# Kernel optimization log

Measured on AMD Instinct MI355X. Metric: run time of the kernel, lower is better.

## Reference

```python
import jax, jax.numpy as jnp
import numpy as np

N_NODES = 100000
N_EDGES = 3200000
IN_CH = 32
OUT_CH = 32
DIM = 2
KSIZE = 3  # per pseudo dimension -> num_kernels = 9


def setup_inputs() -> dict:
    key = jax.random.key(0)
    k1, k2, k3, k4, k5, k6 = jax.random.split(key, 6)
    x = jax.random.normal(k1, (N_NODES, IN_CH), dtype=jnp.float32)
    pseudo = jax.random.uniform(k2, (N_EDGES, DIM), dtype=jnp.float32)
    weight = jax.random.normal(k3, (KSIZE * KSIZE, IN_CH, OUT_CH), dtype=jnp.float32) / np.sqrt(IN_CH)
    root_w = jax.random.normal(k4, (OUT_CH, IN_CH), dtype=jnp.float32) / np.sqrt(IN_CH)
    root_b = jax.random.normal(k5, (OUT_CH,), dtype=jnp.float32) * 0.01
    edge_index = jax.random.randint(k6, (2, N_EDGES), 0, N_NODES, dtype=jnp.int64)
    return {"x": x, "pseudo": pseudo, "weight": weight, "root_w": root_w,
            "root_b": root_b, "edge_index": edge_index}


def _basis(pseudo):
    # degree-1 B-spline (hat) basis per dim, outer product across dims -> [E, K^dim]
    p = jnp.clip(pseudo, 0.0, 1.0)  # [E, dim]
    grid = jnp.linspace(0.0, 1.0, KSIZE, dtype=p.dtype)  # [K]
    dist = jnp.abs(p[:, :, None] - grid[None, None, :])  # [E, dim, K]
    b = jnp.maximum(1.0 - dist * (KSIZE - 1), 0.0)  # [E, dim, K]
    basis = jnp.einsum('ea,eb->eab', b[:, 0], b[:, 1])  # [E, K, K]
    return basis.reshape(p.shape[0], -1)  # [E, K*K]


def reference(x, pseudo, weight, root_w, root_b, edge_index):
    row, col = edge_index[0], edge_index[1]
    basis = _basis(pseudo)  # [E, K]
    # gather + basis-weighted contraction -> per-edge messages [E, out]
    messages = jnp.einsum('ek,ei,kio->eo', basis, x[row], weight)
    out = jnp.zeros((x.shape[0], weight.shape[2]), dtype=x.dtype).at[col].add(messages)
    # mean aggregation: divide by in-degree (clamped to >= 1)
    degree = jnp.zeros((x.shape[0],), dtype=x.dtype).at[col].add(jnp.ones_like(col, dtype=x.dtype))
    out = out / jnp.maximum(degree, 1.0)[:, None]
    # root linear (torch nn.Linear: x @ W.T + b)
    out = out + x @ root_w.T + root_b
    return out
```

## Files before the change

kernel.cpp:

```cpp
#include <hip/hip_runtime.h>
#include <hip/hip_bf16.h>

#define N_NODES 100000
#define N_EDGES 3200000
#define CH 32
#define NK 9
#define KTOT 320
#define RS 328

#define BNODES 128
#define NBUCK ((N_NODES + BNODES - 1) / BNODES)
#define CURS_PAD 16
#define MAXB 4800
#define CHE 12288
#define NCHUNK ((N_EDGES + CHE - 1) / CHE)

typedef __hip_bfloat16 bf16;
typedef unsigned short u16;
typedef __attribute__((ext_vector_type(8))) short bf16x8;
typedef __attribute__((ext_vector_type(4))) float f32x4;

__global__ __launch_bounds__(256) void prep_kernel(const float* __restrict__ x,
                                                   const float* __restrict__ w,
                                                   const float* __restrict__ rw,
                                                   bf16* __restrict__ xb,
                                                   bf16* __restrict__ Bg) {
    int idx = blockIdx.x * 256 + threadIdx.x;
    if (idx < N_NODES * CH / 4) {
        float4 v = ((const float4*)x)[idx];
        union { bf16 h[4]; uint2 u; } pk;
        pk.h[0] = __float2bfloat16(v.x);
        pk.h[1] = __float2bfloat16(v.y);
        pk.h[2] = __float2bfloat16(v.z);
        pk.h[3] = __float2bfloat16(v.w);
        ((uint2*)xb)[idx] = pk.u;
    }
    if (idx < NK * CH * CH) {
        int kk = idx >> 5, o = idx & 31;
        Bg[o * RS + kk] = __float2bfloat16(w[idx]);
    }
    if (idx < CH * CH) {
        int o = idx >> 5, i = idx & 31;
        Bg[o * RS + 288 + i] = __float2bfloat16(rw[idx]);
    }
}

__global__ __launch_bounds__(256) void bhist_kernel(const int* __restrict__ ei_col,
                                                    int* __restrict__ hist) {
    __shared__ int h[NBUCK];
    for (int j = threadIdx.x; j < NBUCK; j += 256) h[j] = 0;
    __syncthreads();
    const int4* c4 = (const int4*)ei_col;
    int stride = gridDim.x * 256;
    for (int e = blockIdx.x * 256 + threadIdx.x; e < N_EDGES / 4; e += stride) {
        int4 v = c4[e];
        atomicAdd(&h[v.x >> 7], 1);
        atomicAdd(&h[v.y >> 7], 1);
        atomicAdd(&h[v.z >> 7], 1);
        atomicAdd(&h[v.w >> 7], 1);
    }
    __syncthreads();
    for (int j = threadIdx.x; j < NBUCK; j += 256)
        if (h[j]) atomicAdd(&hist[j], h[j]);
}

__global__ __launch_bounds__(1024) void bscan_kernel(const int* __restrict__ hist,
                                                     int* __restrict__ bstart,
                                                     int* __restrict__ cursor) {
    __shared__ int s[1024];
    int t = threadIdx.x;
    int a = (2 * t < NBUCK) ? hist[2 * t] : 0;
    int b = (2 * t + 1 < NBUCK) ? hist[2 * t + 1] : 0;
    s[t] = a + b;
    __syncthreads();
    for (int off = 1; off < 1024; off <<= 1) {
        int u = (t >= off) ? s[t - off] : 0;
        __syncthreads();
        s[t] += u;
        __syncthreads();
    }
    int excl = s[t] - (a + b);
    if (2 * t < NBUCK) {
        bstart[2 * t] = excl;
        cursor[2 * t * CURS_PAD] = excl;
    }
    if (2 * t + 1 < NBUCK) {
        bstart[2 * t + 1] = excl + a;
        cursor[(2 * t + 1) * CURS_PAD] = excl + a;
    }
    if (t == 1023) bstart[NBUCK] = s[1023];
}

__global__ __launch_bounds__(1024) void place_kernel(const float* __restrict__ pseudo,
                                                     const int* __restrict__ ei,
                                                     int* __restrict__ cursor,
                                                     uint2* __restrict__ edata) {
    __shared__ int h[NBUCK];
    __shared__ int gb[NBUCK];
    __shared__ int cols[CHE];
    int tid = threadIdx.x;
    int c0 = blockIdx.x * CHE;
    int cend = min(c0 + CHE, N_EDGES);

    for (int j = tid; j < NBUCK; j += 1024) h[j] = 0;
    __syncthreads();
    for (int e = c0 + tid; e < cend; e += 1024) {
        int c = ei[N_EDGES + e];
        cols[e - c0] = c;
        atomicAdd(&h[c >> 7], 1);
    }
    __syncthreads();
    for (int j = tid; j < NBUCK; j += 1024)
        gb[j] = h[j] ? atomicAdd(&cursor[j * CURS_PAD], h[j]) : 0;
    __syncthreads();

    for (int e = c0 + tid; e < cend; e += 1024) {
        int col = cols[e - c0];
        int row = ei[e];
        float2 pp = ((const float2*)pseudo)[e];
        float pa = fminf(fmaxf(pp.x, 0.f), 1.f);
        float pb = fminf(fmaxf(pp.y, 0.f), 1.f);
        int ia = pa < 0.5f ? 0 : 1;
        int ib = pb < 0.5f ? 0 : 1;
        float wa1 = 2.f * (pa - 0.5f * (float)ia);
        float wb1 = 2.f * (pb - 0.5f * (float)ib);
        unsigned qa = (unsigned)(wa1 * 65535.f + 0.5f);
        unsigned qb = (unsigned)(wb1 * 65535.f + 0.5f);
        int pos = atomicAdd(&gb[col >> 7], 1);
        uint2 d;
        d.x = (unsigned)row | ((unsigned)ia << 17) | ((unsigned)ib << 18)
            | ((unsigned)(col & 127) << 20);
        d.y = qa | (qb << 16);
        edata[pos] = d;
    }
}

__global__ __launch_bounds__(256) void bsort_kernel(const int* __restrict__ bstart,
                                                    uint2* __restrict__ edata,
                                                    int* __restrict__ nstart,
                                                    int* __restrict__ ncnt) {
    __shared__ uint2 buf[MAXB];
    __shared__ int h[BNODES];
    __shared__ int cur[BNODES];
    __shared__ int tp[256];
    int tid = threadIdx.x;
    int b = blockIdx.x;
    int e0 = bstart[b], e1 = bstart[b + 1];
    int sz = min(e1 - e0, MAXB);

    if (tid < BNODES) h[tid] = 0;
    for (int j = tid; j < sz; j += 256) buf[j] = edata[e0 + j];
    __syncthreads();
    for (int j = tid; j < sz; j += 256)
        atomicAdd(&h[(buf[j].x >> 20) & 127], 1);
    __syncthreads();
    int v = (tid < BNODES) ? h[tid] : 0;
    tp[tid] = v;
    __syncthreads();
    for (int d = 1; d < 256; d <<= 1) {
        int u = (tid >= d) ? tp[tid - d] : 0;
        __syncthreads();
        tp[tid] += u;
        __syncthreads();
    }
    int excl = tp[tid] - v;
    if (tid < BNODES) {
        cur[tid] = excl;
        int n = b * BNODES + tid;
        if (n < N_NODES) { nstart[n] = e0 + excl; ncnt[n] = v; }
    }
    __syncthreads();
    for (int j = tid; j < sz; j += 256) {
        uint2 r = buf[j];
        unsigned xx = r.x;
        int key = (xx >> 20) & 127;
        int p = atomicAdd(&cur[key], 1);
        float wa1f = (float)(r.y & 0xFFFF) * (1.f / 65535.f);
        float wb1f = (float)(r.y >> 16) * (1.f / 65535.f);
        unsigned wa1b = __float_as_uint(wa1f) >> 16;
        unsigned wb1b = __float_as_uint(wb1f) >> 16;
        uint2 outr;
        outr.x = ((xx & 0x1FFFF) << 6)
               | ((xx & (1u << 17)) << 13)
               | ((xx & (1u << 18)) << 13);
        outr.y = wa1b | (wb1b << 16);
        edata[e0 + p] = outr;
    }
}

__global__ __launch_bounds__(256, 6) void gather_mm_kernel(const bf16* __restrict__ xb,
                                                           const bf16* __restrict__ Bg,
                                                           const float* __restrict__ rb,
                                                           const int* __restrict__ nstart,
                                                           const int* __restrict__ ncnt,
                                                           const uint2* __restrict__ edata,
                                                           float* __restrict__ out) {
    __shared__ __align__(16) bf16 zlds[16 * RS];
    __shared__ __align__(16) bf16 coef[4][16 * 40];
    __shared__ __align__(16) bf16 xt[4][32 * 36];
    int tid = threadIdx.x;
    int wid = tid >> 6;
    int lane = tid & 63;
    int lr = lane & 15, lg = lane >> 4;
    int e31 = lane & 31;
    int n0 = blockIdx.x * 16;
    const char* xbb = (const char*)xb;

    bf16* coefW = coef[wid];
    u16* xtU = (u16*)xt[wid];

    {
        int* cz = (int*)coefW;
        for (int j = lane; j < 16 * 40 / 2; j += 64) cz[j] = 0;
    }

    for (int s = 0; s < 4; ++s) {
        int rr = wid * 4 + s;
        int n = n0 + rr;
        int s0 = nstart[n];
        int dg = ncnt[n];
        f32x4 accL = {0.f, 0.f, 0.f, 0.f};
        f32x4 accH = {0.f, 0.f, 0.f, 0.f};
        int ng = (dg + 31) >> 5;

        for (int g = 0; g < ng; ++g) {
            uint2 rec = edata[s0 + g * 32 + e31];
            bool valid = (g * 32 + e31) < dg;
            float wa1 = __uint_as_float(rec.y << 16);
            float wb1 = __uint_as_float(rec.y & 0xFFFF0000u);
            wa1 = valid ? wa1 : 0.f;
            wb1 = valid ? wb1 : 0.f;
            float wa0 = 1.f - wa1, wb0 = 1.f - wb1;
            unsigned rx = rec.x;
            int ia = (rx >> 30) & 1;
            int ib = (rx >> 31) & 1;
            float A0 = ia ? 0.f : wa0, A1 = ia ? wa0 : wa1, A2 = ia ? wa1 : 0.f;
            float B0 = ib ? 0.f : wb0, B1 = ib ? wb0 : wb1, B2 = ib ? wb1 : 0.f;
            A0 = valid ? A0 : 0.f;
            A1 = valid ? A1 : 0.f;
            A2 = valid ? A2 : 0.f;
            int ro = valid ? (int)(rx & 0x00FFFFC0u) : 0;

            if (lane < 32) {
                coefW[0 * 40 + e31] = __float2bfloat16(A0 * B0);
                coefW[1 * 40 + e31] = __float2bfloat16(A0 * B1);
                coefW[2 * 40 + e31] = __float2bfloat16(A0 * B2);
                coefW[3 * 40 + e31] = __float2bfloat16(A1 * B0);
                coefW[4 * 40 + e31] = __float2bfloat16(A1 * B1);
                coefW[5 * 40 + e31] = __float2bfloat16(A1 * B2);
                coefW[6 * 40 + e31] = __float2bfloat16(A2 * B0);
                coefW[7 * 40 + e31] = __float2bfloat16(A2 * B1);
                coefW[8 * 40 + e31] = __float2bfloat16(A2 * B2);
            }

            int rem = dg - g * 32;
#pragma unroll
            for (int t = 0; t < 2; ++t) {
                int e = 16 * t + (lane >> 2);
                int roe = __shfl(ro, e);
                uint4 v = *(const uint4*)(xbb + roe + (lane & 3) * 16);
                bool vx = e < rem;
                v.x = vx ? v.x : 0u;
                v.y = vx ? v.y : 0u;
                v.z = vx ? v.z : 0u;
                v.w = vx ? v.w : 0u;
                int c0 = (lane & 3) * 8;
                xtU[(c0 + 0) * 36 + e] = (u16)(v.x);
                xtU[(c0 + 1) * 36 + e] = (u16)(v.x >> 16);
                xtU[(c0 + 2) * 36 + e] = (u16)(v.y);
                xtU[(c0 + 3) * 36 + e] = (u16)(v.y >> 16);
                xtU[(c0 + 4) * 36 + e] = (u16)(v.z);
                xtU[(c0 + 5) * 36 + e] = (u16)(v.z >> 16);
                xtU[(c0 + 6) * 36 + e] = (u16)(v.w);
                xtU[(c0 + 7) * 36 + e] = (u16)(v.w >> 16);
            }

            bf16x8 af = *(const bf16x8*)(coefW + lr * 40 + lg * 8);
            const uint2* xlo = (const uint2*)((const char*)xtU + lr * 72 + lg * 16);
            const uint2* xhi = (const uint2*)((const char*)xtU + (lr + 16) * 72 + lg * 16);
            uint2 l0 = xlo[0], l1 = xlo[1];
            uint2 h0 = xhi[0], h1 = xhi[1];
            union UB { unsigned w[4]; bf16x8 v; } bl, bh;
            bl.w[0] = l0.x; bl.w[1] = l0.y; bl.w[2] = l1.x; bl.w[3] = l1.y;
            bh.w[0] = h0.x; bh.w[1] = h0.y; bh.w[2] = h1.x; bh.w[3] = h1.y;
            accL = __builtin_amdgcn_mfma_f32_16x16x32_bf16(af, bl.v, accL, 0, 0, 0);
            accH = __builtin_amdgcn_mfma_f32_16x16x32_bf16(af, bh.v, accH, 0, 0, 0);
        }

        float inv = 1.f / fmaxf((float)dg, 1.f);
#pragma unroll
        for (int r = 0; r < 4; ++r) {
            int p = lg * 4 + r;
            if (p < 9) {
                zlds[rr * RS + p * 32 + lr]      = __float2bfloat16(accL[r] * inv);
                zlds[rr * RS + p * 32 + lr + 16] = __float2bfloat16(accH[r] * inv);
            }
        }
        if (lane < CH) zlds[rr * RS + 288 + lane] = xb[(size_t)n * CH + lane];
    }
    __syncthreads();

    if (wid < 2) {
        const bf16* brow = Bg + (size_t)(lr + wid * 16) * RS;
        f32x4 acc = {0.f, 0.f, 0.f, 0.f};
#pragma unroll
        for (int ks = 0; ks < 10; ++ks) {
            int kk = ks * 32 + lg * 8;
            bf16x8 a = *(const bf16x8*)(zlds + lr * RS + kk);
            bf16x8 b = *(const bf16x8*)(brow + kk);
            acc = __builtin_amdgcn_mfma_f32_16x16x32_bf16(a, b, acc, 0, 0, 0);
        }
        float bias = rb[lr + wid * 16];
#pragma unroll
        for (int r = 0; r < 4; ++r) {
            int n = n0 + lg * 4 + r;
            out[(size_t)n * CH + lr + wid * 16] = acc[r] + bias;
        }
    }
}

extern "C" void kernel_launch(void* const* d_in, const int* in_sizes, int n_in,
                              void* d_out, int out_size, void* d_ws, size_t ws_size,
                              hipStream_t stream) {
    const float* x      = (const float*)d_in[0];
    const float* pseudo = (const float*)d_in[1];
    const float* weight = (const float*)d_in[2];
    const float* root_w = (const float*)d_in[3];
    const float* root_b = (const float*)d_in[4];
    const int*   ei     = (const int*)d_in[5];
    float* out = (float*)d_out;

    int* hist    = (int*)d_ws;
    int* bstart  = hist + 1024;
    int* cursor  = bstart + 1024;
    int* nstart  = cursor + 12544;
    int* ncnt    = nstart + 100032;
    char* basep  = (char*)(ncnt + 100032);
    size_t off   = ((size_t)(basep - (char*)d_ws) + 1023) & ~(size_t)1023;
    uint2* edata = (uint2*)((char*)d_ws + off);
    bf16* xb     = (bf16*)(edata + N_EDGES + 64);
    bf16* Bg     = xb + (size_t)N_NODES * CH;

    hipMemsetAsync(hist, 0, NBUCK * sizeof(int), stream);
    prep_kernel<<<(N_NODES * CH / 4 + 255) / 256, 256, 0, stream>>>(x, weight, root_w, xb, Bg);
    bhist_kernel<<<256, 256, 0, stream>>>(ei + N_EDGES, hist);
    bscan_kernel<<<1, 1024, 0, stream>>>(hist, bstart, cursor);
    place_kernel<<<NCHUNK, 1024, 0, stream>>>(pseudo, ei, cursor, edata);
    bsort_kernel<<<NBUCK, 256, 0, stream>>>(bstart, edata, nstart, ncnt);
    gather_mm_kernel<<<N_NODES / 16, 256, 0, stream>>>(xb, Bg, root_b, nstart, ncnt,
                                                       edata, out);
}
```

Before: 175.8 us.

## Locally sort edges by bucket in place_kernel for coalesced scatter writes

The place kernel now builds a per-chunk bucket histogram, prefix-scans it in shared memory, and writes a bucket-sorted permutation of the chunk's edge indices into shared memory. The output loop then walks edges in bucket order, so consecutive threads write contiguous positions in edata instead of scattering through per-bucket shared atomics. This aims to make the global stores coalesced. In exchange it adds a 1024-wide block scan, re-reads the column and row indices and pseudo values through a gather, and shrinks the chunk size to fit the new shared arrays, which means more blocks and more global cursor atomics.

```diff
diff --git a/kernel.cpp b/kernel.cpp
--- a/kernel.cpp
+++ b/kernel.cpp
@@ -12,7 +12,7 @@
 #define NBUCK ((N_NODES + BNODES - 1) / BNODES)
 #define CURS_PAD 16
 #define MAXB 4800
-#define CHE 12288
+#define CHE 8192
 #define NCHUNK ((N_EDGES + CHE - 1) / CHE)
 
 typedef __hip_bfloat16 bf16;
@@ -96,26 +96,48 @@
                                                      int* __restrict__ cursor,
                                                      uint2* __restrict__ edata) {
     __shared__ int h[NBUCK];
+    __shared__ int loff[NBUCK];
     __shared__ int gb[NBUCK];
-    __shared__ int cols[CHE];
+    __shared__ int cur[NBUCK];
+    __shared__ unsigned inv[CHE];
+    __shared__ int tps[1024];
     int tid = threadIdx.x;
     int c0 = blockIdx.x * CHE;
     int cend = min(c0 + CHE, N_EDGES);
+    int sz = cend - c0;
 
     for (int j = tid; j < NBUCK; j += 1024) h[j] = 0;
     __syncthreads();
+    for (int e = c0 + tid; e < cend; e += 1024)
+        atomicAdd(&h[ei[N_EDGES + e] >> 7], 1);
+    __syncthreads();
+    int v = (tid < NBUCK) ? h[tid] : 0;
+    tps[tid] = v;
+    __syncthreads();
+    for (int d = 1; d < 1024; d <<= 1) {
+        int u = (tid >= d) ? tps[tid - d] : 0;
+        __syncthreads();
+        tps[tid] += u;
+        __syncthreads();
+    }
+    if (tid < NBUCK) {
+        int excl = tps[tid] - v;
+        loff[tid] = excl;
+        cur[tid] = excl;
+        gb[tid] = v ? atomicAdd(&cursor[tid * CURS_PAD], v) : 0;
+    }
+    __syncthreads();
     for (int e = c0 + tid; e < cend; e += 1024) {
-        int c = ei[N_EDGES + e];
-        cols[e - c0] = c;
-        atomicAdd(&h[c >> 7], 1);
-    }
-    __syncthreads();
-    for (int j = tid; j < NBUCK; j += 1024)
-        gb[j] = h[j] ? atomicAdd(&cursor[j * CURS_PAD], h[j]) : 0;
-    __syncthreads();
-
-    for (int e = c0 + tid; e < cend; e += 1024) {
-        int col = cols[e - c0];
+        int b = ei[N_EDGES + e] >> 7;
+        int p = atomicAdd(&cur[b], 1);
+        inv[p] = (unsigned)(e - c0) | ((unsigned)b << 13);
+    }
+    __syncthreads();
+    for (int q = tid; q < sz; q += 1024) {
+        unsigned u = inv[q];
+        int e = c0 + (int)(u & 8191);
+        int b = (int)(u >> 13);
+        int col = ei[N_EDGES + e];
         int row = ei[e];
         float2 pp = ((const float2*)pseudo)[e];
         float pa = fminf(fmaxf(pp.x, 0.f), 1.f);
@@ -126,12 +148,11 @@
         float wb1 = 2.f * (pb - 0.5f * (float)ib);
         unsigned qa = (unsigned)(wa1 * 65535.f + 0.5f);
         unsigned qb = (unsigned)(wb1 * 65535.f + 0.5f);
-        int pos = atomicAdd(&gb[col >> 7], 1);
         uint2 d;
         d.x = (unsigned)row | ((unsigned)ia << 17) | ((unsigned)ib << 18)
             | ((unsigned)(col & 127) << 20);
         d.y = qa | (qb << 16);
-        edata[pos] = d;
+        edata[gb[b] + (q - loff[b])] = d;
     }
 }
 
```

New measurement: 198.2 us. +12.7%, slower.
